# Kernel optimization log

Hardware: AMD Instinct MI355X
Metric: run time of the kernel (lower is better)

## Reference

```python
import jax, jax.numpy as jnp
import numpy as np

N, C, K = 300000, 64, 27  # active voxels, channels, 3^3 kernel offsets


def sparse_conv(x, nbr, mask, W, b):
    """MinkowskiConvolution as gather -> GEMM -> accumulate.
    x: [N, C] features; nbr: [N, K] int32 neighbor index per kernel offset;
    mask: [N, K] bool validity; W: [K, C, C]; b: [C].
    out[i] = b + sum_k mask[i,k] * x[nbr[i,k]] @ W[k]
    Scans over the K=27 fixed kernel offsets so only an [N, C] gathered
    buffer is live at a time (never materializes [N, K, C]).
    """
    def step(acc, kin):
        Wk, nk, mk = kin
        g = jnp.where(mk[:, None], x[nk], jnp.zeros((), x.dtype))  # [N, C] gather
        return acc + g @ Wk, None

    acc0 = jnp.zeros_like(x) + b
    out, _ = jax.lax.scan(step, acc0, (W, nbr.T, mask.T))
    return out


def setup_inputs() -> dict:
    key = jax.random.key(0)
    ks = jax.random.split(key, 7)
    features = jax.random.normal(ks[0], (N, C), dtype=jnp.float32)
    neighbor_idx = jax.random.randint(ks[1], (N, K), 0, N, dtype=jnp.int32)
    neighbor_mask = jax.random.uniform(ks[2], (N, K)) < 0.6  # variable neighbor counts
    scale = 1.0 / np.sqrt(K * C)
    W0 = jax.random.normal(ks[3], (K, C, C), dtype=jnp.float32) * scale
    b0 = jax.random.normal(ks[4], (C,), dtype=jnp.float32) * 0.01
    W1 = jax.random.normal(ks[5], (K, C, C), dtype=jnp.float32) * scale
    b1 = jax.random.normal(ks[6], (C,), dtype=jnp.float32) * 0.01
    return {
        "features": features,
        "neighbor_idx": neighbor_idx,
        "neighbor_mask": neighbor_mask,
        "W0": W0, "b0": b0, "W1": W1, "b1": b1,
    }


def reference(features, neighbor_idx, neighbor_mask, W0, b0, W1, b1):
    # conv0 -> ReLU -> conv1 -> residual add (stride=1, shared kernel map)
    out = sparse_conv(features, neighbor_idx, neighbor_mask, W0, b0)
    out = jax.nn.relu(out)
    out = sparse_conv(out, neighbor_idx, neighbor_mask, W1, b1)
    return out + features
```

## Files before the change

### kernel.cpp

```cpp
#include <hip/hip_runtime.h>
#include <hip/hip_bf16.h>
#include <stdint.h>

typedef __bf16 bf16x8 __attribute__((ext_vector_type(8)));
typedef float f32x4 __attribute__((ext_vector_type(4)));
typedef unsigned short u16x4 __attribute__((ext_vector_type(4)));

__device__ __forceinline__ unsigned short f2bf(float f) {
    union { float f; uint32_t u; } v; v.f = f;
    uint32_t u = v.u;
    return (unsigned short)((u + 0x7fffu + ((u >> 16) & 1u)) >> 16);
}

__device__ __forceinline__ float bf2f(unsigned short b) {
    union { uint32_t u; float f; } v; v.u = ((uint32_t)b) << 16;
    return v.f;
}

__global__ __launch_bounds__(256) void prep_x(const f32x4* __restrict__ x,
                                              u16x4* __restrict__ xb, int n4, int n4tot) {
    int t = blockIdx.x * 256 + threadIdx.x;
    if (t < n4) {
        f32x4 v = x[t];
        u16x4 o;
        o.x = f2bf(v.x); o.y = f2bf(v.y); o.z = f2bf(v.z); o.w = f2bf(v.w);
        xb[t] = o;
    } else if (t < n4tot) {
        u16x4 z = {0, 0, 0, 0};
        xb[t] = z;
    }
}

__global__ void zero_row(unsigned short* __restrict__ p, long off) {
    p[off + threadIdx.x] = 0;
}

__global__ __launch_bounds__(256) void prep_w(const float* __restrict__ W,
                                              unsigned short* __restrict__ Wf, int K) {
    int k = blockIdx.x;
    unsigned short* Wfk = Wf + (size_t)k * 4096;
    const float* Wk = W + (size_t)k * 4096;
    for (int idx = threadIdx.x; idx < 4096; idx += 256) {
        int j   = idx & 7;
        int l   = (idx >> 3) & 63;
        int c2h = idx >> 9;
        int ct  = c2h >> 1, h = c2h & 1;
        int ci  = h * 32 + (l >> 4) * 8 + j;
        int co  = ct * 16 + (l & 15);
        Wfk[idx] = (k < K) ? f2bf(Wk[ci * 64 + co]) : (unsigned short)0;
    }
}

__global__ void detect_mask(const unsigned int* __restrict__ m, int* __restrict__ flag) {
    __shared__ int s_not_int, s_not_f32;
    if (threadIdx.x == 0) { s_not_int = 0; s_not_f32 = 0; }
    __syncthreads();
    unsigned int w = m[threadIdx.x];
    if (w > 1u) s_not_int = 1;
    if (w != 0u && w != 0x3f800000u) s_not_f32 = 1;
    __syncthreads();
    if (threadIdx.x == 0) *flag = s_not_int ? (s_not_f32 ? 1 : 2) : 0;
}

template <int IOFF>
__device__ __forceinline__ bf16x8 gl16(const unsigned short* base, unsigned voff) {
    bf16x8 r;
    asm volatile("global_load_dwordx4 %0, %1, %2 offset:%c3"
                 : "=v"(r) : "v"(voff), "s"(base), "i"(IOFF));
    return r;
}

struct Slot { bf16x8 f[8]; };

template <int NW>
__device__ __forceinline__ void waitv(Slot& s) {
    asm volatile("s_waitcnt vmcnt(%c8)"
                 : "+v"(s.f[0]), "+v"(s.f[1]), "+v"(s.f[2]), "+v"(s.f[3]),
                   "+v"(s.f[4]), "+v"(s.f[5]), "+v"(s.f[6]), "+v"(s.f[7])
                 : "i"(NW));
    __builtin_amdgcn_sched_barrier(0);
}

__device__ __forceinline__ void gload_lds16(const unsigned short* g, unsigned short* l) {
    __builtin_amdgcn_global_load_lds(
        (const __attribute__((address_space(1))) void*)(const void*)g,
        (__attribute__((address_space(3))) void*)(void*)l, 16, 0, 0);
}

template <int MODE>
__global__ __launch_bounds__(256, 2) void conv_mfma(
    const unsigned short* __restrict__ xb,
    const int* __restrict__ nbr,
    const void* __restrict__ maskp,
    const int* __restrict__ flagp,
    const unsigned short* __restrict__ Wf,
    const float* __restrict__ bias,
    const unsigned short* __restrict__ residb,
    void* __restrict__ outp,
    int N, int K)
{
    __shared__ unsigned short Wlds[16384];

    const int tid = threadIdx.x;
    const int wv  = tid >> 6;
    const int l   = tid & 63;
    const int lr  = l & 15;
    const int lg  = l >> 4;
    const int wavebase = blockIdx.x * 256 + wv * 64;

    const int myrow = wavebase + l;
    const int mr = myrow < N ? myrow : N - 1;

    unsigned mbits = 0;
    {
        const int flag = *flagp;
        long moff = (long)mr * K;
        if (flag == 1) {
            const unsigned char* mp = (const unsigned char*)maskp + moff;
#pragma unroll
            for (int k = 0; k < 27; ++k) mbits |= (mp[k] ? 1u : 0u) << k;
        } else if (flag == 0) {
            const int* mp = (const int*)maskp + moff;
#pragma unroll
            for (int k = 0; k < 27; ++k) mbits |= (mp[k] ? 1u : 0u) << k;
        } else {
            const float* mp = (const float*)maskp + moff;
#pragma unroll
            for (int k = 0; k < 27; ++k) mbits |= ((mp[k] != 0.f) ? 1u : 0u) << k;
        }
    }

    unsigned o[28];
    {
        const int* nrow = nbr + (long)mr * K;
#pragma unroll
        for (int k = 0; k < 27; ++k) {
            unsigned g = ((mbits >> k) & 1u) ? (unsigned)nrow[k] : (unsigned)N;
            o[k] = g * 128u;
        }
        o[27] = (unsigned)N * 128u;
    }

    const int bpa0 = (0 * 16 + lr) * 4;
    const int bpa1 = (1 * 16 + lr) * 4;
    const int bpa2 = (2 * 16 + lr) * 4;
    const int bpa3 = (3 * 16 + lr) * 4;
    const unsigned chk = (unsigned)(lg << 4);

    f32x4 acc[4][4] = {};
    Slot pipe[2];
    bf16x8 Bf[8];

#define STAGE(P) do { \
    const unsigned short* _src = Wf + (size_t)(P) * 8192 + wv * 2048 + (l << 3); \
    unsigned short* _dst = &Wlds[((P) & 1) * 8192 + wv * 2048]; \
    _Pragma("unroll") \
    for (int _s = 0; _s < 4; ++_s) \
        gload_lds16(_src + _s * 512, _dst + _s * 512); \
    asm volatile("" ::: "memory"); \
} while (0)

#define GISSUE(J) do { \
    unsigned _b0 = (unsigned)__builtin_amdgcn_ds_bpermute(bpa0, (int)o[J]) + chk; \
    unsigned _b1 = (unsigned)__builtin_amdgcn_ds_bpermute(bpa1, (int)o[J]) + chk; \
    unsigned _b2 = (unsigned)__builtin_amdgcn_ds_bpermute(bpa2, (int)o[J]) + chk; \
    unsigned _b3 = (unsigned)__builtin_amdgcn_ds_bpermute(bpa3, (int)o[J]) + chk; \
    Slot& _s = pipe[(J) & 1]; \
    _s.f[0] = gl16<0 >(xb, _b0); _s.f[1] = gl16<64>(xb, _b0); \
    _s.f[2] = gl16<0 >(xb, _b1); _s.f[3] = gl16<64>(xb, _b1); \
    _s.f[4] = gl16<0 >(xb, _b2); _s.f[5] = gl16<64>(xb, _b2); \
    _s.f[6] = gl16<0 >(xb, _b3); _s.f[7] = gl16<64>(xb, _b3); \
} while (0)

#define BLOAD(J) do { \
    const unsigned short* _wl = &Wlds[(((J) >> 1) & 1) * 8192 + ((J) & 1) * 4096]; \
    _Pragma("unroll") \
    for (int _c = 0; _c < 8; ++_c) \
        Bf[_c] = *(const bf16x8*)(_wl + _c * 512 + l * 8); \
} while (0)

#define MFMA16(J) do { \
    Slot& _s = pipe[(J) & 1]; \
    _Pragma("unroll") \
    for (int ct = 0; ct < 4; ++ct) { \
        _Pragma("unroll") \
        for (int at = 0; at < 4; ++at) { \
            acc[at][ct] = __builtin_amdgcn_mfma_f32_16x16x32_bf16(_s.f[at * 2],     Bf[ct * 2],     acc[at][ct], 0, 0, 0); \
            acc[at][ct] = __builtin_amdgcn_mfma_f32_16x16x32_bf16(_s.f[at * 2 + 1], Bf[ct * 2 + 1], acc[at][ct], 0, 0, 0); \
        } \
    } \
} while (0)

#define FENCE() do { \
    asm volatile("s_waitcnt vmcnt(16)" ::: "memory"); \
    __builtin_amdgcn_sched_barrier(0); \
    __builtin_amdgcn_s_barrier(); \
    __builtin_amdgcn_sched_barrier(0); \
} while (0)

#define STEP(J, NW) do { BLOAD(J); waitv<NW>(pipe[(J) & 1]); MFMA16(J); } while (0)

#define PHASE(PH1, K0) do { \
    STAGE(PH1); \
    STEP(K0, 12);       GISSUE((K0) + 2); \
    STEP((K0) + 1, 12); GISSUE((K0) + 3); \
    FENCE(); \
} while (0)

    STAGE(0);
    GISSUE(0); GISSUE(1);
    asm volatile("s_waitcnt vmcnt(16)" ::: "memory");
    __builtin_amdgcn_sched_barrier(0);
    __builtin_amdgcn_s_barrier();
    __builtin_amdgcn_sched_barrier(0);

    PHASE(1, 0);   PHASE(2, 2);   PHASE(3, 4);   PHASE(4, 6);
    PHASE(5, 8);   PHASE(6, 10);  PHASE(7, 12);  PHASE(8, 14);
    PHASE(9, 16);  PHASE(10, 18); PHASE(11, 20); PHASE(12, 22);
    PHASE(13, 24);
    STEP(26, 8);
    STEP(27, 0);

#pragma unroll
    for (int at = 0; at < 4; ++at) {
#pragma unroll
        for (int ct = 0; ct < 4; ++ct) {
            int col = ct * 16 + lr;
            float bv = bias[col];
#pragma unroll
            for (int rg = 0; rg < 4; ++rg) {
                int row = wavebase + at * 16 + lg * 4 + rg;
                if (row < N) {
                    long oo = (long)row * 64 + col;
                    float v = acc[at][ct][rg] + bv;
                    if (MODE == 0) {
                        ((unsigned short*)outp)[oo] = f2bf(v > 0.f ? v : 0.f);
                    } else {
                        ((float*)outp)[oo] = v + bf2f(residb[oo]);
                    }
                }
            }
        }
    }

#undef STAGE
#undef GISSUE
#undef BLOAD
#undef MFMA16
#undef FENCE
#undef STEP
#undef PHASE
}

static inline size_t align256(size_t x) { return (x + 255) & ~(size_t)255; }

extern "C" void kernel_launch(void* const* d_in, const int* in_sizes, int n_in,
                              void* d_out, int out_size, void* d_ws, size_t ws_size,
                              hipStream_t stream) {
    const float* x    = (const float*)d_in[0];
    const int*   nbr  = (const int*)d_in[1];
    const void*  mask = d_in[2];
    const float* W0   = (const float*)d_in[3];
    const float* b0   = (const float*)d_in[4];
    const float* W1   = (const float*)d_in[5];
    const float* b1   = (const float*)d_in[6];

    const int NC = in_sizes[0];
    const int N  = NC / 64;
    const int K  = in_sizes[1] / N;
    const int KP = 28;

    char* ws = (char*)d_ws;
    size_t xb_bytes = (size_t)(NC + 64) * 2;
    size_t wt_bytes = (size_t)KP * 4096 * 2;
    size_t xb_off   = 0;
    size_t hb_off   = xb_off + align256(xb_bytes);
    size_t wt0_off  = hb_off + align256(xb_bytes);
    size_t wt1_off  = wt0_off + align256(wt_bytes);
    size_t flag_off = wt1_off + align256(wt_bytes);

    unsigned short* xb  = (unsigned short*)(ws + xb_off);
    unsigned short* hb  = (unsigned short*)(ws + hb_off);
    unsigned short* wf0 = (unsigned short*)(ws + wt0_off);
    unsigned short* wf1 = (unsigned short*)(ws + wt1_off);
    int* flag           = (int*)(ws + flag_off);

    int n4 = NC / 4;
    int n4tot = n4 + 16;
    prep_x<<<(n4tot + 255) / 256, 256, 0, stream>>>((const f32x4*)x, (u16x4*)xb, n4, n4tot);
    zero_row<<<1, 64, 0, stream>>>(hb, (long)NC);
    prep_w<<<KP, 256, 0, stream>>>(W0, wf0, K);
    prep_w<<<KP, 256, 0, stream>>>(W1, wf1, K);
    detect_mask<<<1, 1024, 0, stream>>>((const unsigned int*)mask, flag);

    int nblocks = (N + 255) / 256;
    conv_mfma<0><<<nblocks, 256, 0, stream>>>(xb, nbr, mask, flag, wf0, b0, nullptr, hb, N, K);
    conv_mfma<1><<<nblocks, 256, 0, stream>>>(hb, nbr, mask, flag, wf1, b1, xb, d_out, N, K);
}
```

Baseline: 339.4 us.

## Drop padded 28th kernel offset, prefetch bpermute addresses, add priority and nontemporal hints

Removes the padded dummy 28th kernel offset, so the tail of the pipeline does 27 gather+MFMA steps instead of 28 and stages only half the final weight tile. Lane-permuted gather addresses are now computed two steps ahead (GPERM) so ds_bpermute latency overlaps MFMA work. MFMA blocks are bracketed with s_setprio, and mask/neighbor/residual loads and output stores use nontemporal hints to reduce cache pollution. The risks are the reworked tail wait counts and higher register pressure from the prefetched address arrays.

```diff
diff --git a/kernel.cpp b/kernel.cpp
--- a/kernel.cpp
+++ b/kernel.cpp
@@ -36,7 +36,7 @@
 }
 
 __global__ __launch_bounds__(256) void prep_w(const float* __restrict__ W,
-                                              unsigned short* __restrict__ Wf, int K) {
+                                              unsigned short* __restrict__ Wf) {
     int k = blockIdx.x;
     unsigned short* Wfk = Wf + (size_t)k * 4096;
     const float* Wk = W + (size_t)k * 4096;
@@ -47,7 +47,7 @@
         int ct  = c2h >> 1, h = c2h & 1;
         int ci  = h * 32 + (l >> 4) * 8 + j;
         int co  = ct * 16 + (l & 15);
-        Wfk[idx] = (k < K) ? f2bf(Wk[ci * 64 + co]) : (unsigned short)0;
+        Wfk[idx] = f2bf(Wk[ci * 64 + co]);
     }
 }
 
@@ -118,27 +118,30 @@
         if (flag == 1) {
             const unsigned char* mp = (const unsigned char*)maskp + moff;
 #pragma unroll
-            for (int k = 0; k < 27; ++k) mbits |= (mp[k] ? 1u : 0u) << k;
+            for (int k = 0; k < 27; ++k)
+                mbits |= (__builtin_nontemporal_load(mp + k) ? 1u : 0u) << k;
         } else if (flag == 0) {
             const int* mp = (const int*)maskp + moff;
 #pragma unroll
-            for (int k = 0; k < 27; ++k) mbits |= (mp[k] ? 1u : 0u) << k;
+            for (int k = 0; k < 27; ++k)
+                mbits |= (__builtin_nontemporal_load(mp + k) ? 1u : 0u) << k;
         } else {
             const float* mp = (const float*)maskp + moff;
 #pragma unroll
-            for (int k = 0; k < 27; ++k) mbits |= ((mp[k] != 0.f) ? 1u : 0u) << k;
+            for (int k = 0; k < 27; ++k)
+                mbits |= ((__builtin_nontemporal_load(mp + k) != 0.f) ? 1u : 0u) << k;
         }
     }
 
-    unsigned o[28];
+    unsigned o[27];
     {
         const int* nrow = nbr + (long)mr * K;
 #pragma unroll
         for (int k = 0; k < 27; ++k) {
-            unsigned g = ((mbits >> k) & 1u) ? (unsigned)nrow[k] : (unsigned)N;
+            int nv = __builtin_nontemporal_load(nrow + k);
+            unsigned g = ((mbits >> k) & 1u) ? (unsigned)nv : (unsigned)N;
             o[k] = g * 128u;
         }
-        o[27] = (unsigned)N * 128u;
     }
 
     const int bpa0 = (0 * 16 + lr) * 4;
@@ -150,6 +153,7 @@
     f32x4 acc[4][4] = {};
     Slot pipe[2];
     bf16x8 Bf[8];
+    unsigned bpr[2][4];
 
 #define STAGE(P) do { \
     const unsigned short* _src = Wf + (size_t)(P) * 8192 + wv * 2048 + (l << 3); \
@@ -160,16 +164,28 @@
     asm volatile("" ::: "memory"); \
 } while (0)
 
+#define STAGE1(P) do { \
+    const unsigned short* _src = Wf + (size_t)(P) * 8192 + wv * 1024 + (l << 3); \
+    unsigned short* _dst = &Wlds[((P) & 1) * 8192 + wv * 1024]; \
+    _Pragma("unroll") \
+    for (int _s = 0; _s < 2; ++_s) \
+        gload_lds16(_src + _s * 512, _dst + _s * 512); \
+    asm volatile("" ::: "memory"); \
+} while (0)
+
+#define GPERM(J) do { if ((J) <= 26) { \
+    bpr[(J) & 1][0] = (unsigned)__builtin_amdgcn_ds_bpermute(bpa0, (int)o[(J)]) + chk; \
+    bpr[(J) & 1][1] = (unsigned)__builtin_amdgcn_ds_bpermute(bpa1, (int)o[(J)]) + chk; \
+    bpr[(J) & 1][2] = (unsigned)__builtin_amdgcn_ds_bpermute(bpa2, (int)o[(J)]) + chk; \
+    bpr[(J) & 1][3] = (unsigned)__builtin_amdgcn_ds_bpermute(bpa3, (int)o[(J)]) + chk; \
+} } while (0)
+
 #define GISSUE(J) do { \
-    unsigned _b0 = (unsigned)__builtin_amdgcn_ds_bpermute(bpa0, (int)o[J]) + chk; \
-    unsigned _b1 = (unsigned)__builtin_amdgcn_ds_bpermute(bpa1, (int)o[J]) + chk; \
-    unsigned _b2 = (unsigned)__builtin_amdgcn_ds_bpermute(bpa2, (int)o[J]) + chk; \
-    unsigned _b3 = (unsigned)__builtin_amdgcn_ds_bpermute(bpa3, (int)o[J]) + chk; \
     Slot& _s = pipe[(J) & 1]; \
-    _s.f[0] = gl16<0 >(xb, _b0); _s.f[1] = gl16<64>(xb, _b0); \
-    _s.f[2] = gl16<0 >(xb, _b1); _s.f[3] = gl16<64>(xb, _b1); \
-    _s.f[4] = gl16<0 >(xb, _b2); _s.f[5] = gl16<64>(xb, _b2); \
-    _s.f[6] = gl16<0 >(xb, _b3); _s.f[7] = gl16<64>(xb, _b3); \
+    _s.f[0] = gl16<0 >(xb, bpr[(J) & 1][0]); _s.f[1] = gl16<64>(xb, bpr[(J) & 1][0]); \
+    _s.f[2] = gl16<0 >(xb, bpr[(J) & 1][1]); _s.f[3] = gl16<64>(xb, bpr[(J) & 1][1]); \
+    _s.f[4] = gl16<0 >(xb, bpr[(J) & 1][2]); _s.f[5] = gl16<64>(xb, bpr[(J) & 1][2]); \
+    _s.f[6] = gl16<0 >(xb, bpr[(J) & 1][3]); _s.f[7] = gl16<64>(xb, bpr[(J) & 1][3]); \
 } while (0)
 
 #define BLOAD(J) do { \
@@ -181,6 +197,7 @@
 
 #define MFMA16(J) do { \
     Slot& _s = pipe[(J) & 1]; \
+    __builtin_amdgcn_s_setprio(1); \
     _Pragma("unroll") \
     for (int ct = 0; ct < 4; ++ct) { \
         _Pragma("unroll") \
@@ -189,10 +206,11 @@
             acc[at][ct] = __builtin_amdgcn_mfma_f32_16x16x32_bf16(_s.f[at * 2 + 1], Bf[ct * 2 + 1], acc[at][ct], 0, 0, 0); \
         } \
     } \
-} while (0)
-
-#define FENCE() do { \
-    asm volatile("s_waitcnt vmcnt(16)" ::: "memory"); \
+    __builtin_amdgcn_s_setprio(0); \
+} while (0)
+
+#define FENCE(NW) do { \
+    asm volatile("s_waitcnt vmcnt(%c0)" :: "i"(NW) : "memory"); \
     __builtin_amdgcn_sched_barrier(0); \
     __builtin_amdgcn_s_barrier(); \
     __builtin_amdgcn_sched_barrier(0); \
@@ -202,13 +220,15 @@
 
 #define PHASE(PH1, K0) do { \
     STAGE(PH1); \
-    STEP(K0, 12);       GISSUE((K0) + 2); \
-    STEP((K0) + 1, 12); GISSUE((K0) + 3); \
-    FENCE(); \
+    STEP(K0, 12);       GISSUE((K0) + 2); GPERM((K0) + 4); \
+    STEP((K0) + 1, 12); GISSUE((K0) + 3); GPERM((K0) + 5); \
+    FENCE(16); \
 } while (0)
 
     STAGE(0);
+    GPERM(0); GPERM(1);
     GISSUE(0); GISSUE(1);
+    GPERM(2); GPERM(3);
     asm volatile("s_waitcnt vmcnt(16)" ::: "memory");
     __builtin_amdgcn_sched_barrier(0);
     __builtin_amdgcn_s_barrier();
@@ -217,9 +237,11 @@
     PHASE(1, 0);   PHASE(2, 2);   PHASE(3, 4);   PHASE(4, 6);
     PHASE(5, 8);   PHASE(6, 10);  PHASE(7, 12);  PHASE(8, 14);
     PHASE(9, 16);  PHASE(10, 18); PHASE(11, 20); PHASE(12, 22);
-    PHASE(13, 24);
-    STEP(26, 8);
-    STEP(27, 0);
+    STAGE1(13);
+    STEP(24, 10); GISSUE(26);
+    STEP(25, 10);
+    FENCE(8);
+    STEP(26, 0);
 
 #pragma unroll
     for (int at = 0; at < 4; ++at) {
@@ -234,9 +256,11 @@
                     long oo = (long)row * 64 + col;
                     float v = acc[at][ct][rg] + bv;
                     if (MODE == 0) {
-                        ((unsigned short*)outp)[oo] = f2bf(v > 0.f ? v : 0.f);
+                        __builtin_nontemporal_store(f2bf(v > 0.f ? v : 0.f),
+                                                    (unsigned short*)outp + oo);
                     } else {
-                        ((float*)outp)[oo] = v + bf2f(residb[oo]);
+                        unsigned short rb = __builtin_nontemporal_load(residb + oo);
+                        __builtin_nontemporal_store(v + bf2f(rb), (float*)outp + oo);
                     }
                 }
             }
@@ -244,6 +268,8 @@
     }
 
 #undef STAGE
+#undef STAGE1
+#undef GPERM
 #undef GISSUE
 #undef BLOAD
 #undef MFMA16
@@ -268,11 +294,10 @@
     const int NC = in_sizes[0];
     const int N  = NC / 64;
     const int K  = in_sizes[1] / N;
-    const int KP = 28;
 
     char* ws = (char*)d_ws;
     size_t xb_bytes = (size_t)(NC + 64) * 2;
-    size_t wt_bytes = (size_t)KP * 4096 * 2;
+    size_t wt_bytes = (size_t)28 * 4096 * 2;
     size_t xb_off   = 0;
     size_t hb_off   = xb_off + align256(xb_bytes);
     size_t wt0_off  = hb_off + align256(xb_bytes);
@@ -289,8 +314,8 @@
     int n4tot = n4 + 16;
     prep_x<<<(n4tot + 255) / 256, 256, 0, stream>>>((const f32x4*)x, (u16x4*)xb, n4, n4tot);
     zero_row<<<1, 64, 0, stream>>>(hb, (long)NC);
-    prep_w<<<KP, 256, 0, stream>>>(W0, wf0, K);
-    prep_w<<<KP, 256, 0, stream>>>(W1, wf1, K);
+    prep_w<<<27, 256, 0, stream>>>(W0, wf0);
+    prep_w<<<27, 256, 0, stream>>>(W1, wf1);
     detect_mask<<<1, 1024, 0, stream>>>((const unsigned int*)mask, flag);
 
     int nblocks = (N + 255) / 256;
```

Measured after the change: 416.7 us. +22.8%, slower.
